# Performance work log

Hardware: AMD Instinct MI355X
Metric: run time of the kernel (lower is better)

The kernel has to match this reference:

```python
import jax, jax.numpy as jnp
import numpy as np

B, S, DIM, H = 2, 4096, 512, 8
HD = DIM // H
SCALE = HD ** -0.5
EPS = 1e-5


def setup_inputs() -> dict:
    key = jax.random.key(0)
    ks = jax.random.split(key, 7)
    std = DIM ** -0.5
    return {
        "x": jax.random.normal(ks[0], (B, S, DIM), dtype=jnp.float32),
        "ln_gamma": jnp.ones((DIM,), jnp.float32),
        "ln_beta": jnp.zeros((DIM,), jnp.float32),
        "w_q": jax.random.normal(ks[1], (DIM, DIM), jnp.float32) * std,
        "w_k": jax.random.normal(ks[2], (DIM, DIM), jnp.float32) * std,
        "w_v": jax.random.normal(ks[3], (DIM, DIM), jnp.float32) * std,
        "w_fc": jax.random.normal(ks[4], (DIM, DIM), jnp.float32) * std,
    }


def reference(x, ln_gamma, ln_beta, w_q, w_k, w_v, w_fc):
    # LayerNorm over last dim
    mu = jnp.mean(x, axis=-1, keepdims=True)
    var = jnp.var(x, axis=-1, keepdims=True)
    xn = (x - mu) * jax.lax.rsqrt(var + EPS) * ln_gamma + ln_beta
    # QKV projections (torch Linear: y = x @ W.T), split into heads -> [B,H,S,HD]
    q = jnp.einsum('bsd,ed->bse', xn, w_q).reshape(B, S, H, HD).transpose(0, 2, 1, 3)
    k = jnp.einsum('bsd,ed->bse', xn, w_k).reshape(B, S, H, HD).transpose(0, 2, 1, 3)
    v = jnp.einsum('bsd,ed->bse', xn, w_v).reshape(B, S, H, HD).transpose(0, 2, 1, 3)
    # scores [B,H,S,S]
    attn = jnp.einsum('bhqd,bhkd->bhqk', q, k) * SCALE
    attn = jax.nn.softmax(attn, axis=-1)
    # dropout is identity in eval mode
    out = jnp.einsum('bhqk,bhkd->bhqd', attn, v)
    out = out.transpose(0, 2, 1, 3).reshape(B, S, DIM)
    return jnp.einsum('bsd,ed->bse', out, w_fc)
```

## Files before the change

### kernel.cpp

```cpp
#include <hip/hip_runtime.h>
#include <cstdint>
#include <cstddef>

typedef unsigned short u16;
typedef unsigned int   u32;
typedef __bf16 bf16x8 __attribute__((ext_vector_type(8)));
typedef float  f32x4  __attribute__((ext_vector_type(4)));
typedef float  f32x16 __attribute__((ext_vector_type(16)));
typedef u16    u16x8  __attribute__((ext_vector_type(8)));
typedef u16    u16x4  __attribute__((ext_vector_type(4)));
typedef u32    u32x2  __attribute__((ext_vector_type(2)));
typedef u32    u32x4  __attribute__((ext_vector_type(4)));

#define DI __device__ __forceinline__

constexpr int SEQ = 4096;
constexpr int DIM = 512;
constexpr int NH  = 8;
constexpr int HD  = 64;
constexpr float ATT_C1 = 0.125f * 1.44269504088896340736f;

DI u16 f2bf(float f) {
  u32 u = __builtin_bit_cast(u32, f);
  u += 0x7fffu + ((u >> 16) & 1u);
  return (u16)(u >> 16);
}

DI u32 pk2(float hi, float lo) {
  u32 uh = __builtin_bit_cast(u32, hi) + 0x8000u;
  u32 ul = __builtin_bit_cast(u32, lo) + 0x8000u;
  return __builtin_amdgcn_perm(uh, ul, 0x07060302u);
}

DI u32 cvtpk(float a, float b) {
  u32 r;
  asm("v_cvt_pk_bf16_f32 %0, %1, %2" : "=v"(r) : "v"(a), "v"(b));
  return r;
}

DI void plswap(u32& a, u32& b) {
  asm("v_permlane32_swap_b32 %0, %1" : "+v"(a), "+v"(b));
}

__global__ __launch_bounds__(256) void wconv_kernel(
    const float* __restrict__ wq, const float* __restrict__ wk,
    const float* __restrict__ wv, const float* __restrict__ wfc,
    u16* __restrict__ Wb)
{
  const int idx  = blockIdx.x * 256 + threadIdx.x;
  const int base = idx * 8;
  const int mat  = base >> 18;
  const int off  = base & (512 * 512 - 1);
  const float* src = (mat == 0) ? wq : (mat == 1) ? wk : (mat == 2) ? wv : wfc;
  const float4 a = *(const float4*)(src + off);
  const float4 b = *(const float4*)(src + off + 4);
  u32x4 o = { pk2(a.y, a.x), pk2(a.w, a.z), pk2(b.y, b.x), pk2(b.w, b.z) };
  *(u32x4*)(Wb + base) = o;
}

__global__ __launch_bounds__(256) void ln_cast_kernel(
    const float* __restrict__ x, const float* __restrict__ gamma,
    const float* __restrict__ beta, u16* __restrict__ xn)
{
  const int row  = blockIdx.x * 4 + (threadIdx.x >> 6);
  const int lane = threadIdx.x & 63;
  const float* xr = x + (size_t)row * DIM + lane * 8;
  const float4 a = *(const float4*)xr;
  const float4 b = *(const float4*)(xr + 4);
  float s = a.x + a.y + a.z + a.w + b.x + b.y + b.z + b.w;
  float q = a.x*a.x + a.y*a.y + a.z*a.z + a.w*a.w
          + b.x*b.x + b.y*b.y + b.z*b.z + b.w*b.w;
#pragma unroll
  for (int m = 1; m < 64; m <<= 1) {
    s += __shfl_xor(s, m, 64);
    q += __shfl_xor(q, m, 64);
  }
  const float mu = s * (1.0f / DIM);
  const float rs = rsqrtf(q * (1.0f / DIM) - mu * mu + 1e-5f);
  const float4 g0 = *(const float4*)(gamma + lane * 8);
  const float4 g1 = *(const float4*)(gamma + lane * 8 + 4);
  const float4 e0 = *(const float4*)(beta + lane * 8);
  const float4 e1 = *(const float4*)(beta + lane * 8 + 4);
  const float v0 = (a.x - mu) * rs * g0.x + e0.x;
  const float v1 = (a.y - mu) * rs * g0.y + e0.y;
  const float v2 = (a.z - mu) * rs * g0.z + e0.z;
  const float v3 = (a.w - mu) * rs * g0.w + e0.w;
  const float v4 = (b.x - mu) * rs * g1.x + e1.x;
  const float v5 = (b.y - mu) * rs * g1.y + e1.y;
  const float v6 = (b.z - mu) * rs * g1.z + e1.z;
  const float v7 = (b.w - mu) * rs * g1.w + e1.w;
  u32x4 o = { pk2(v1, v0), pk2(v3, v2), pk2(v5, v4), pk2(v7, v6) };
  *(u32x4*)(xn + (size_t)row * DIM + lane * 8) = o;
}

template<int MODE>
__global__ __launch_bounds__(256, 2) void gemm_kernel(
    const u16* __restrict__ A, const u16* __restrict__ Wb,
    u16* __restrict__ Qo, u16* __restrict__ Ko, u16* __restrict__ Vt,
    float* __restrict__ Co)
{
  __shared__ u16 As[128][72];
  __shared__ u16 Bs[128][72];
  const int m0 = blockIdx.y * 128, n0 = blockIdx.x * 128;
  const int t = threadIdx.x, wave = t >> 6, lane = t & 63;
  const int quad = lane >> 4, l15 = lane & 15;
  const int wm = wave >> 1, wn = wave & 1;
  const u16* Wsrc;
  if (MODE == 0) {
    const int mat = n0 >> 9;
    Wsrc = Wb + (size_t)mat * 512 * 512 + (size_t)(n0 & 511) * DIM;
  } else {
    Wsrc = Wb + (size_t)3 * 512 * 512 + (size_t)n0 * DIM;
  }

  f32x4 acc[4][4];
#pragma unroll
  for (int i = 0; i < 4; i++)
#pragma unroll
    for (int j = 0; j < 4; j++)
#pragma unroll
      for (int r = 0; r < 4; r++) acc[i][j][r] = 0.0f;

  for (int kk = 0; kk < DIM; kk += 64) {
    __syncthreads();
#pragma unroll
    for (int it = 0; it < 4; it++) {
      const int c4 = t + it * 256;
      const int r = c4 >> 3, off = (c4 & 7) * 8;
      *(u16x8*)&As[r][off] =
          *(const u16x8*)(A + (size_t)(m0 + r) * DIM + kk + off);
      *(u16x8*)&Bs[r][off] =
          *(const u16x8*)(Wsrc + (size_t)r * DIM + kk + off);
    }
    __syncthreads();
#pragma unroll
    for (int kx = 0; kx < 2; kx++) {
      bf16x8 af[4], bfr[4];
#pragma unroll
      for (int i = 0; i < 4; i++)
        af[i] = *(const bf16x8*)&As[wm * 64 + i * 16 + l15][kx * 32 + quad * 8];
#pragma unroll
      for (int j = 0; j < 4; j++)
        bfr[j] = *(const bf16x8*)&Bs[wn * 64 + j * 16 + l15][kx * 32 + quad * 8];
#pragma unroll
      for (int i = 0; i < 4; i++)
#pragma unroll
        for (int j = 0; j < 4; j++)
          acc[i][j] = __builtin_amdgcn_mfma_f32_16x16x32_bf16(
              af[i], bfr[j], acc[i][j], 0, 0, 0);
    }
  }

  if (MODE == 1) {
#pragma unroll
    for (int i = 0; i < 4; i++) {
      const int m = m0 + wm * 64 + i * 16 + quad * 4;
#pragma unroll
      for (int j = 0; j < 4; j++) {
        const int n = n0 + wn * 64 + j * 16 + l15;
#pragma unroll
        for (int r = 0; r < 4; r++)
          Co[(size_t)(m + r) * DIM + n] = acc[i][j][r];
      }
    }
  } else {
    const int mat = n0 >> 9;
    const float qs = (mat == 0) ? ATT_C1 : 1.0f;
#pragma unroll
    for (int i = 0; i < 4; i++) {
      const int m = m0 + wm * 64 + i * 16 + quad * 4;
      const int b = m >> 12, s = m & 4095;
#pragma unroll
      for (int j = 0; j < 4; j++) {
        const int ng = (n0 & 511) + wn * 64 + j * 16 + l15;
        const int h = ng >> 6, d = ng & 63;
        if (mat < 2) {
          u16* dst = (mat == 0 ? Qo : Ko) +
                     ((size_t)(b * NH + h) * SEQ) * HD + d;
#pragma unroll
          for (int r = 0; r < 4; r++)
            dst[(size_t)(s + r) * HD] = f2bf(acc[i][j][r] * qs);
        } else {
          u32x2 w;
          w[0] = pk2(acc[i][j][1], acc[i][j][0]);
          w[1] = pk2(acc[i][j][3], acc[i][j][2]);
          *(u32x2*)&Vt[((size_t)(b * NH + h) * HD + d) * SEQ + s] = w;
        }
      }
    }
  }
}

__global__ __launch_bounds__(256, 2) void attn_kernel(
    const u16* __restrict__ Q, const u16* __restrict__ K,
    const u16* __restrict__ Vt, u16* __restrict__ O)
{
  __shared__ u16 Kl[128][72];
  __shared__ u16 Vl[64][136];
  const int flat = blockIdx.x + 32 * blockIdx.y;
  const int slot = flat >> 3;
  const int bh = (flat & 7) * 2 + (slot & 1);
  const int qt = slot >> 1;
  const int b = bh >> 3, h = bh & 7;
  const int t = threadIdx.x, wave = t >> 6, lane = t & 63;
  const int l31 = lane & 31, hf = lane >> 5;
  const u16* Qb = Q + (size_t)bh * SEQ * HD;
  const u16* Kb = K + (size_t)bh * SEQ * HD;
  const u16* Vb = Vt + (size_t)bh * HD * SEQ;
  const int qw = qt * 128 + wave * 32;

  bf16x8 bq[4];
#pragma unroll
  for (int kk = 0; kk < 4; kk++)
    bq[kk] = *(const bf16x8*)(Qb + (size_t)(qw + l31) * HD + kk * 16 + hf * 8);

  f32x16 oacc[2];
#pragma unroll
  for (int mt = 0; mt < 2; mt++)
#pragma unroll
    for (int r = 0; r < 16; r++) oacc[mt][r] = 0.0f;
  float lrun = 0.0f;

  const int st_r  = t >> 3,  st_off = (t & 7) * 8;
  const int st_d  = t >> 4,  st_o2  = (t & 15) * 8;

  u16x8 kst[4], vst[4];
#pragma unroll
  for (int it = 0; it < 4; it++) {
    const int c4 = t + it * 256;
    const int r = c4 >> 3, off = (c4 & 7) * 8;
    kst[it] = *(const u16x8*)(Kb + (size_t)r * HD + off);
    const int d = c4 >> 4, o2 = (c4 & 15) * 8;
    vst[it] = *(const u16x8*)(Vb + (size_t)d * SEQ + o2);
  }

  for (int kc = 0; kc < SEQ; kc += 128) {
    __syncthreads();
#pragma unroll
    for (int it = 0; it < 4; it++) {
      const int c4 = t + it * 256;
      const int r = c4 >> 3, off = (c4 & 7) * 8;
      *(u16x8*)&Kl[r][off] = kst[it];
      const int d = c4 >> 4, o2 = (c4 & 15) * 8;
      *(u16x8*)&Vl[d][o2] = vst[it];
    }
    __syncthreads();
    if (kc + 128 < SEQ) {
#pragma unroll
      for (int it = 0; it < 4; it++) {
        const int c4 = t + it * 256;
        const int r = c4 >> 3, off = (c4 & 7) * 8;
        kst[it] = *(const u16x8*)(Kb + (size_t)(kc + 128 + r) * HD + off);
        const int d = c4 >> 4, o2 = (c4 & 15) * 8;
        vst[it] = *(const u16x8*)(Vb + (size_t)d * SEQ + kc + 128 + o2);
      }
    }

#pragma unroll
    for (int mt = 0; mt < 4; mt++) {
      f32x16 s;
#pragma unroll
      for (int r = 0; r < 16; r++) s[r] = 0.0f;
      __builtin_amdgcn_s_setprio(1);
#pragma unroll
      for (int kk = 0; kk < 4; kk++) {
        const bf16x8 ka =
            *(const bf16x8*)&Kl[mt * 32 + l31][kk * 16 + hf * 8];
        s = __builtin_amdgcn_mfma_f32_32x32x16_bf16(ka, bq[kk], s, 0, 0, 0);
      }
      __builtin_amdgcn_s_setprio(0);

      float e[16];
#pragma unroll
      for (int r = 0; r < 16; r++) e[r] = __builtin_amdgcn_exp2f(s[r]);
      lrun += (((e[0] + e[1]) + (e[2] + e[3])) +
               ((e[4] + e[5]) + (e[6] + e[7]))) +
              (((e[8] + e[9]) + (e[10] + e[11])) +
               ((e[12] + e[13]) + (e[14] + e[15])));

      u32 a0 = cvtpk(e[0],  e[1]),  a1 = cvtpk(e[2],  e[3]);
      u32 a2 = cvtpk(e[4],  e[5]),  a3 = cvtpk(e[6],  e[7]);
      plswap(a0, a2); plswap(a1, a3);
      u32 c0 = cvtpk(e[8],  e[9]),  c1 = cvtpk(e[10], e[11]);
      u32 c2 = cvtpk(e[12], e[13]), c3 = cvtpk(e[14], e[15]);
      plswap(c0, c2); plswap(c1, c3);
      u32x4 f0v = { a0, a1, a2, a3 };
      u32x4 f1v = { c0, c1, c2, c3 };
      const bf16x8 p0 = __builtin_bit_cast(bf16x8, f0v);
      const bf16x8 p1 = __builtin_bit_cast(bf16x8, f1v);

      __builtin_amdgcn_s_setprio(1);
#pragma unroll
      for (int mt2 = 0; mt2 < 2; mt2++) {
        const bf16x8 va0 =
            *(const bf16x8*)&Vl[mt2 * 32 + l31][(mt * 2 + 0) * 16 + hf * 8];
        oacc[mt2] = __builtin_amdgcn_mfma_f32_32x32x16_bf16(
            va0, p0, oacc[mt2], 0, 0, 0);
        const bf16x8 va1 =
            *(const bf16x8*)&Vl[mt2 * 32 + l31][(mt * 2 + 1) * 16 + hf * 8];
        oacc[mt2] = __builtin_amdgcn_mfma_f32_32x32x16_bf16(
            va1, p1, oacc[mt2], 0, 0, 0);
      }
      __builtin_amdgcn_s_setprio(0);
    }
  }

  const float lt = lrun + __shfl_xor(lrun, 32, 64);
  const float inv = 1.0f / lt;
  const int s = qw + l31;
  u16* Ob = O + ((size_t)(b * SEQ + s)) * DIM + h * HD;
#pragma unroll
  for (int mt2 = 0; mt2 < 2; mt2++)
#pragma unroll
    for (int g = 0; g < 4; g++) {
      u32x2 w;
      w[0] = pk2(oacc[mt2][g * 4 + 1] * inv, oacc[mt2][g * 4 + 0] * inv);
      w[1] = pk2(oacc[mt2][g * 4 + 3] * inv, oacc[mt2][g * 4 + 2] * inv);
      *(u32x2*)&Ob[mt2 * 32 + g * 8 + hf * 4] = w;
    }
}

extern "C" void kernel_launch(void* const* d_in, const int* in_sizes, int n_in,
                              void* d_out, int out_size, void* d_ws,
                              size_t ws_size, hipStream_t stream)
{
  const float* x     = (const float*)d_in[0];
  const float* gamma = (const float*)d_in[1];
  const float* beta  = (const float*)d_in[2];
  const float* wq    = (const float*)d_in[3];
  const float* wk    = (const float*)d_in[4];
  const float* wv    = (const float*)d_in[5];
  const float* wfc   = (const float*)d_in[6];
  float* out = (float*)d_out;

  char* ws = (char*)d_ws;
  u16* xn = (u16*)(ws);
  u16* Qb = (u16*)(ws + ((size_t)8  << 20));
  u16* Kb = (u16*)(ws + ((size_t)16 << 20));
  u16* Vt = (u16*)(ws + ((size_t)24 << 20));
  u16* Ob = (u16*)(ws + ((size_t)32 << 20));
  u16* Wb = (u16*)(ws + ((size_t)40 << 20));

  wconv_kernel<<<512, 256, 0, stream>>>(wq, wk, wv, wfc, Wb);
  ln_cast_kernel<<<2048, 256, 0, stream>>>(x, gamma, beta, xn);
  gemm_kernel<0><<<dim3(12, 64), 256, 0, stream>>>(xn, Wb, Qb, Kb, Vt, nullptr);
  attn_kernel<<<dim3(32, 16), 256, 0, stream>>>(Qb, Kb, Vt, Ob);
  gemm_kernel<1><<<dim3(4, 64), 256, 0, stream>>>(
      Ob, Wb, nullptr, nullptr, nullptr, out);
}
```

Measured before the change: 200.4 us.

## Split attention KV loop across two wave groups with LDS reduction

Each attention block now has 512 threads in two groups of four waves. Each group handles the same 128 queries but walks alternate 128-key chunks, using its own LDS staging buffers. At the end, group 1 writes its partial O accumulators and row sums to shared memory and group 0 adds them before normalising and storing. This split-K over keys doubles the waves available per query tile to hide latency. It costs more LDS per block, an extra reduction phase, and tighter register limits from the new launch bounds.

```diff
diff --git a/kernel.cpp b/kernel.cpp
--- a/kernel.cpp
+++ b/kernel.cpp
@@ -191,23 +191,30 @@
   }
 }
 
-__global__ __launch_bounds__(256, 2) void attn_kernel(
+__global__ __launch_bounds__(512, 4) void attn_kernel(
     const u16* __restrict__ Q, const u16* __restrict__ K,
     const u16* __restrict__ Vt, u16* __restrict__ O)
 {
-  __shared__ u16 Kl[128][72];
-  __shared__ u16 Vl[64][136];
+  __shared__ __align__(16) char smem[71680];
   const int flat = blockIdx.x + 32 * blockIdx.y;
   const int slot = flat >> 3;
   const int bh = (flat & 7) * 2 + (slot & 1);
   const int qt = slot >> 1;
   const int b = bh >> 3, h = bh & 7;
-  const int t = threadIdx.x, wave = t >> 6, lane = t & 63;
+  const int t = threadIdx.x;
+  const int wave = t >> 6, lane = t & 63;
+  const int grp = t >> 8;
+  const int qwave = wave & 3;
+  const int tg = t & 255;
   const int l31 = lane & 31, hf = lane >> 5;
+
+  u16 (*Kl)[72]  = (u16 (*)[72]) (smem + grp * 35840);
+  u16 (*Vl)[136] = (u16 (*)[136])(smem + grp * 35840 + 18432);
+
   const u16* Qb = Q + (size_t)bh * SEQ * HD;
   const u16* Kb = K + (size_t)bh * SEQ * HD;
   const u16* Vb = Vt + (size_t)bh * HD * SEQ;
-  const int qw = qt * 128 + wave * 32;
+  const int qw = qt * 128 + qwave * 32;
 
   bf16x8 bq[4];
 #pragma unroll
@@ -221,38 +228,36 @@
     for (int r = 0; r < 16; r++) oacc[mt][r] = 0.0f;
   float lrun = 0.0f;
 
-  const int st_r  = t >> 3,  st_off = (t & 7) * 8;
-  const int st_d  = t >> 4,  st_o2  = (t & 15) * 8;
-
+  const int kc0 = grp * 128;
   u16x8 kst[4], vst[4];
 #pragma unroll
   for (int it = 0; it < 4; it++) {
-    const int c4 = t + it * 256;
+    const int c4 = tg + it * 256;
     const int r = c4 >> 3, off = (c4 & 7) * 8;
-    kst[it] = *(const u16x8*)(Kb + (size_t)r * HD + off);
+    kst[it] = *(const u16x8*)(Kb + (size_t)(kc0 + r) * HD + off);
     const int d = c4 >> 4, o2 = (c4 & 15) * 8;
-    vst[it] = *(const u16x8*)(Vb + (size_t)d * SEQ + o2);
-  }
-
-  for (int kc = 0; kc < SEQ; kc += 128) {
+    vst[it] = *(const u16x8*)(Vb + (size_t)d * SEQ + kc0 + o2);
+  }
+
+  for (int kc = kc0; kc < SEQ; kc += 256) {
     __syncthreads();
 #pragma unroll
     for (int it = 0; it < 4; it++) {
-      const int c4 = t + it * 256;
+      const int c4 = tg + it * 256;
       const int r = c4 >> 3, off = (c4 & 7) * 8;
       *(u16x8*)&Kl[r][off] = kst[it];
       const int d = c4 >> 4, o2 = (c4 & 15) * 8;
       *(u16x8*)&Vl[d][o2] = vst[it];
     }
     __syncthreads();
-    if (kc + 128 < SEQ) {
+    if (kc + 256 < SEQ) {
 #pragma unroll
       for (int it = 0; it < 4; it++) {
-        const int c4 = t + it * 256;
+        const int c4 = tg + it * 256;
         const int r = c4 >> 3, off = (c4 & 7) * 8;
-        kst[it] = *(const u16x8*)(Kb + (size_t)(kc + 128 + r) * HD + off);
+        kst[it] = *(const u16x8*)(Kb + (size_t)(kc + 256 + r) * HD + off);
         const int d = c4 >> 4, o2 = (c4 & 15) * 8;
-        vst[it] = *(const u16x8*)(Vb + (size_t)d * SEQ + kc + 128 + o2);
+        vst[it] = *(const u16x8*)(Vb + (size_t)d * SEQ + kc + 256 + o2);
       }
     }
 
@@ -305,19 +310,47 @@
     }
   }
 
-  const float lt = lrun + __shfl_xor(lrun, 32, 64);
-  const float inv = 1.0f / lt;
-  const int s = qw + l31;
-  u16* Ob = O + ((size_t)(b * SEQ + s)) * DIM + h * HD;
-#pragma unroll
-  for (int mt2 = 0; mt2 < 2; mt2++)
-#pragma unroll
-    for (int g = 0; g < 4; g++) {
-      u32x2 w;
-      w[0] = pk2(oacc[mt2][g * 4 + 1] * inv, oacc[mt2][g * 4 + 0] * inv);
-      w[1] = pk2(oacc[mt2][g * 4 + 3] * inv, oacc[mt2][g * 4 + 2] * inv);
-      *(u32x2*)&Ob[mt2 * 32 + g * 8 + hf * 4] = w;
-    }
+  __syncthreads();
+  f32x4 (*Rbuf)[8][64] = (f32x4 (*)[8][64])smem;
+  float (*Lbuf)[64]    = (float (*)[64])(smem + 32768);
+  if (grp == 1) {
+#pragma unroll
+    for (int mt2 = 0; mt2 < 2; mt2++)
+#pragma unroll
+      for (int gi = 0; gi < 4; gi++) {
+        f32x4 w;
+#pragma unroll
+        for (int r = 0; r < 4; r++) w[r] = oacc[mt2][gi * 4 + r];
+        Rbuf[qwave][mt2 * 4 + gi][lane] = w;
+      }
+    Lbuf[qwave][lane] = lrun;
+  }
+  __syncthreads();
+  if (grp == 0) {
+#pragma unroll
+    for (int mt2 = 0; mt2 < 2; mt2++)
+#pragma unroll
+      for (int gi = 0; gi < 4; gi++) {
+        const f32x4 w = Rbuf[qwave][mt2 * 4 + gi][lane];
+#pragma unroll
+        for (int r = 0; r < 4; r++) oacc[mt2][gi * 4 + r] += w[r];
+      }
+    lrun += Lbuf[qwave][lane];
+
+    const float lt = lrun + __shfl_xor(lrun, 32, 64);
+    const float inv = 1.0f / lt;
+    const int s = qw + l31;
+    u16* Ob = O + ((size_t)(b * SEQ + s)) * DIM + h * HD;
+#pragma unroll
+    for (int mt2 = 0; mt2 < 2; mt2++)
+#pragma unroll
+      for (int g = 0; g < 4; g++) {
+        u32x2 w;
+        w[0] = pk2(oacc[mt2][g * 4 + 1] * inv, oacc[mt2][g * 4 + 0] * inv);
+        w[1] = pk2(oacc[mt2][g * 4 + 3] * inv, oacc[mt2][g * 4 + 2] * inv);
+        *(u32x2*)&Ob[mt2 * 32 + g * 8 + hf * 4] = w;
+      }
+  }
 }
 
 extern "C" void kernel_launch(void* const* d_in, const int* in_sizes, int n_in,
@@ -344,7 +377,7 @@
   wconv_kernel<<<512, 256, 0, stream>>>(wq, wk, wv, wfc, Wb);
   ln_cast_kernel<<<2048, 256, 0, stream>>>(x, gamma, beta, xn);
   gemm_kernel<0><<<dim3(12, 64), 256, 0, stream>>>(xn, Wb, Qb, Kb, Vt, nullptr);
-  attn_kernel<<<dim3(32, 16), 256, 0, stream>>>(Qb, Kb, Vt, Ob);
+  attn_kernel<<<dim3(32, 16), 512, 0, stream>>>(Qb, Kb, Vt, Ob);
   gemm_kernel<1><<<dim3(4, 64), 256, 0, stream>>>(
       Ob, Wb, nullptr, nullptr, nullptr, out);
 }
```

After: 288.0 us. 43.7% more time.
